# Performance work log

Measured on AMD Instinct MI355X. Metric: run time of the kernel, lower is better.

Reference implementation:

```python
import jax, jax.numpy as jnp
import numpy as np
import math

INPUT_DIM = 1024
DIM_K = 1024
DIM_V = 1024
B, N = 4, 2048

def setup_inputs() -> dict:
    key = jax.random.key(0)
    ks = jax.random.split(key, 7)
    s = 1.0 / math.sqrt(INPUT_DIM)
    return {
        'x':  jax.random.normal(ks[0], (B, N, INPUT_DIM), dtype=jnp.float32),
        'Wq': jax.random.uniform(ks[1], (DIM_K, INPUT_DIM), jnp.float32, -s, s),
        'bq': jax.random.uniform(ks[2], (DIM_K,), jnp.float32, -s, s),
        'Wk': jax.random.uniform(ks[3], (DIM_K, INPUT_DIM), jnp.float32, -s, s),
        'bk': jax.random.uniform(ks[4], (DIM_K,), jnp.float32, -s, s),
        'Wv': jax.random.uniform(ks[5], (DIM_V, INPUT_DIM), jnp.float32, -s, s),
        'bv': jax.random.uniform(ks[6], (DIM_V,), jnp.float32, -s, s),
    }

def reference(x, Wq, bq, Wk, bk, Wv, bv):
    norm_fact = 1.0 / math.sqrt(DIM_K)
    # torch Linear: y = x @ W.T + b
    Q = jnp.einsum('bnd,kd->bnk', x, Wq) + bq  # [B,N,dim_k]
    K = jnp.einsum('bnd,kd->bnk', x, Wk) + bk  # [B,N,dim_k]
    V = jnp.einsum('bnd,vd->bnv', x, Wv) + bv  # [B,N,dim_v]
    scores = jnp.einsum('bqk,bnk->bqn', Q, K)  # [B,N,N]
    # NOTE: original code applies softmax FIRST, then scales by norm_fact
    atten = jax.nn.softmax(scores, axis=-1) * norm_fact
    return jnp.einsum('bqn,bnv->bqv', atten, V)  # [B,N,dim_v]
```

## Files before the change

kernel.cpp:

```cpp
#include <hip/hip_runtime.h>


typedef _Float16 hfx8 __attribute__((ext_vector_type(8)));
typedef _Float16 hfx4 __attribute__((ext_vector_type(4)));
typedef float fx4 __attribute__((ext_vector_type(4)));

__device__ __forceinline__ void load_lds16(const void* g, void* l) {
    __builtin_amdgcn_global_load_lds(
        (const __attribute__((address_space(1))) void*)g,
        (__attribute__((address_space(3))) void*)l, 16, 0, 0);
}

template <int N> __device__ __forceinline__ void vmwait() {
    if constexpr (N == 8) asm volatile("s_waitcnt vmcnt(8)" ::: "memory");
    else if constexpr (N == 4) asm volatile("s_waitcnt vmcnt(4)" ::: "memory");
    else asm volatile("s_waitcnt vmcnt(0)" ::: "memory");
}

__device__ __forceinline__ void xcd_remap(int& x, int& y, int& z) {
    const int gx = gridDim.x, gy = gridDim.y;
    const int lin = blockIdx.x + gx * (blockIdx.y + gy * blockIdx.z);
    const int cpx = (gx * gy * gridDim.z) >> 3;
    const int w = (lin & 7) * cpx + (lin >> 3);
    x = w % gx;
    y = (w / gx) % gy;
    z = w / (gx * gy);
}

__global__ __launch_bounds__(256) void convx_kernel(
    const float4* __restrict__ in, _Float16* __restrict__ out)
{
    const int i = blockIdx.x * 256 + threadIdx.x;
    float4 v = in[i];
    hfx4 h;
    h[0] = (_Float16)v.x; h[1] = (_Float16)v.y;
    h[2] = (_Float16)v.z; h[3] = (_Float16)v.w;
    *(hfx4*)&out[(long)i * 4] = h;
}

__global__ __launch_bounds__(256) void convw3_kernel(
    const float4* __restrict__ w0, const float4* __restrict__ w1, const float4* __restrict__ w2,
    _Float16* __restrict__ o0, _Float16* __restrict__ o1, _Float16* __restrict__ o2)
{
    const int wsel = blockIdx.x >> 10;
    const float4* in = wsel == 0 ? w0 : (wsel == 1 ? w1 : w2);
    _Float16* out = wsel == 0 ? o0 : (wsel == 1 ? o1 : o2);
    const int i = (blockIdx.x & 1023) * 256 + threadIdx.x;
    float4 v = in[i];
    hfx4 h;
    h[0] = (_Float16)v.x; h[1] = (_Float16)v.y;
    h[2] = (_Float16)v.z; h[3] = (_Float16)v.w;
    *(hfx4*)&out[(long)i * 4] = h;
}

template <int OMODE>
__global__ __launch_bounds__(256, 4) void gemm2(
    const _Float16* __restrict__ A,
    const _Float16* __restrict__ Bq, const _Float16* __restrict__ Bk, const _Float16* __restrict__ Bv,
    const float* __restrict__ bq, const float* __restrict__ bk, const float* __restrict__ bv,
    float* __restrict__ outF, _Float16* __restrict__ oQ, _Float16* __restrict__ oK, _Float16* __restrict__ oV,
    int K, int lda, int ldb, int ldc, float alpha,
    long sAz, long sBz, long sCz)
{
    constexpr int BM = 128, BN = 128, BK = 32;
    constexpr int LPT = 4;

    __shared__ __attribute__((aligned(16))) _Float16 lds[2][(BM + BN) * BK];

    int bx, by, z;
    xcd_remap(bx, by, z);

    A += (long)z * sAz;
    const _Float16* B = (OMODE == 1) ? (z == 0 ? Bq : (z == 1 ? Bk : Bv))
                                     : Bq + (long)z * sBz;

    const int tid = threadIdx.x;
    const int lane = tid & 63;
    const int wv = tid >> 6;
    const int wr = wv >> 1, wc = wv & 1;
    const int lr = lane & 15, lk = lane >> 4;

    const long m0 = (long)by * BM;
    const long n0 = (long)bx * BN;

    fx4 acc[4][4] = {};

    auto STAGE = [&](int kt, int b) {
#pragma unroll
        for (int i = 0; i < LPT; ++i) {
            const int c = i * 256 + tid;
            if (i < 2) {
                const int row = c >> 2, slot = c & 3;
                load_lds16(A + (m0 + row) * (long)lda + kt + ((slot ^ ((row >> 1) & 3)) << 3),
                           &lds[b][row * 32 + slot * 8]);
            } else {
                const int c2 = c - 512;
                const int row = c2 >> 2, slot = c2 & 3;
                load_lds16(B + (n0 + row) * (long)ldb + kt + ((slot ^ ((row >> 1) & 3)) << 3),
                           &lds[b][BM * BK + row * 32 + slot * 8]);
            }
        }
    };

    const int NT = K / BK;
    STAGE(0, 0);
    STAGE(BK, 1);
    vmwait<4>();
    __builtin_amdgcn_s_barrier();
    __builtin_amdgcn_sched_barrier(0);

    const int rA0 = wr * 64 + lr;
    const int rB0 = wc * 64 + lr;
    const int eA = (((rA0 >> 1) & 3) << 3);
    const int eB = (((rB0 >> 1) & 3) << 3);

    for (int t = 0; t < NT; ++t) {
        const _Float16* LA = &lds[t & 1][0];
        const _Float16* LB = LA + BM * BK;

        hfx8 bfr[4];
#pragma unroll
        for (int nf = 0; nf < 4; ++nf)
            bfr[nf] = *(const hfx8*)&LB[(rB0 + nf * 16) * BK + ((lk * 8) ^ eB)];

#pragma unroll
        for (int q = 0; q < 4; ++q) {
            hfx8 afr = *(const hfx8*)&LA[(rA0 + q * 16) * BK + ((lk * 8) ^ eA)];
            __builtin_amdgcn_s_setprio(1);
#pragma unroll
            for (int nf = 0; nf < 4; ++nf)
                acc[q][nf] = __builtin_amdgcn_mfma_f32_16x16x32_f16(
                    afr, bfr[nf], acc[q][nf], 0, 0, 0);
            __builtin_amdgcn_s_setprio(0);
        }

        __builtin_amdgcn_s_barrier();
        if (t + 2 < NT) {
            STAGE((t + 2) * BK, t & 1);
            vmwait<4>();
        } else {
            vmwait<0>();
        }
        __builtin_amdgcn_s_barrier();
        __builtin_amdgcn_sched_barrier(0);
    }

#pragma unroll
    for (int mf = 0; mf < 4; ++mf) {
#pragma unroll
        for (int nf = 0; nf < 4; ++nf) {
            const long row0 = m0 + wr * 64 + mf * 16 + lk * 4;
            const long col = n0 + wc * 64 + nf * 16 + lr;
            if constexpr (OMODE == 0) {
                float* oz = outF + (long)z * sCz;
#pragma unroll
                for (int j = 0; j < 4; ++j)
                    oz[(row0 + j) * (long)ldc + col] = alpha * acc[mf][nf][j];
            } else {
                if (z == 0) {
                    const float bb = bq[col];
#pragma unroll
                    for (int j = 0; j < 4; ++j)
                        oQ[(row0 + j) * 1024 + col] = (_Float16)(acc[mf][nf][j] + bb);
                } else if (z == 1) {
                    const float bb = bk[col];
#pragma unroll
                    for (int j = 0; j < 4; ++j)
                        oK[(row0 + j) * 1024 + col] = (_Float16)(acc[mf][nf][j] + bb);
                } else {
                    const float bb = bv[col];
                    hfx4 pk;
#pragma unroll
                    for (int j = 0; j < 4; ++j) pk[j] = (_Float16)(acc[mf][nf][j] + bb);
                    *(hfx4*)&oV[((row0 >> 11) * 1024 + col) * 2048 + (row0 & 2047)] = pk;
                }
            }
        }
    }
}

__global__ __launch_bounds__(256) void softmax_kernel(float* __restrict__ S)
{
    const long row = blockIdx.x;
    float* r = S + row * 2048;
    const int t = threadIdx.x;

    float4 v0 = *(const float4*)&r[t * 4];
    float4 v1 = *(const float4*)&r[1024 + t * 4];
    float v[8] = {v0.x, v0.y, v0.z, v0.w, v1.x, v1.y, v1.z, v1.w};

    float mx = v[0];
#pragma unroll
    for (int j = 1; j < 8; ++j) mx = fmaxf(mx, v[j]);
#pragma unroll
    for (int o = 32; o; o >>= 1) mx = fmaxf(mx, __shfl_xor(mx, o, 64));

    __shared__ float redm[4];
    __shared__ float reds[4];
    const int w = t >> 6;
    if ((t & 63) == 0) redm[w] = mx;
    __syncthreads();
    mx = fmaxf(fmaxf(redm[0], redm[1]), fmaxf(redm[2], redm[3]));

    float e[8];
    float s = 0.f;
#pragma unroll
    for (int j = 0; j < 8; ++j) {
        e[j] = __expf(v[j] - mx);
        s += e[j];
    }
#pragma unroll
    for (int o = 32; o; o >>= 1) s += __shfl_xor(s, o, 64);
    if ((t & 63) == 0) reds[w] = s;
    __syncthreads();
    s = reds[0] + reds[1] + reds[2] + reds[3];

    const float inv = 1.0f / s;
    hfx4 p0, p1;
#pragma unroll
    for (int j = 0; j < 4; ++j) {
        p0[j] = (_Float16)(e[j] * inv);
        p1[j] = (_Float16)(e[4 + j] * inv);
    }
    _Float16* pr = (_Float16*)r;
    *(hfx4*)&pr[t * 4] = p0;
    *(hfx4*)&pr[1024 + t * 4] = p1;
}

extern "C" void kernel_launch(void* const* d_in, const int* in_sizes, int n_in,
                              void* d_out, int out_size, void* d_ws, size_t ws_size,
                              hipStream_t stream)
{
    const float* x  = (const float*)d_in[0];
    const float* Wq = (const float*)d_in[1];
    const float* bq = (const float*)d_in[2];
    const float* Wk = (const float*)d_in[3];
    const float* bk = (const float*)d_in[4];
    const float* Wv = (const float*)d_in[5];
    const float* bv = (const float*)d_in[6];
    float* out = (float*)d_out;

    _Float16* xs  = (_Float16*)d_ws;
    _Float16* Wqh = xs + 8192ull * 1024;
    _Float16* Wkh = Wqh + 1024ull * 1024;
    _Float16* Wvh = Wkh + 1024ull * 1024;
    _Float16* Qp  = Wvh + 1024ull * 1024;
    _Float16* Ks  = Qp + 8192ull * 1024;
    _Float16* Vt  = Ks + 8192ull * 1024;
    float* S      = (float*)(Vt + 4ull * 1024 * 2048);

    dim3 blk(256);

    convx_kernel<<<8192, blk, 0, stream>>>((const float4*)x, xs);
    convw3_kernel<<<3072, blk, 0, stream>>>(
        (const float4*)Wq, (const float4*)Wk, (const float4*)Wv, Wqh, Wkh, Wvh);

    gemm2<1><<<dim3(8, 64, 3), blk, 0, stream>>>(
        xs, Wqh, Wkh, Wvh, bq, bk, bv,
        nullptr, Qp, Ks, Vt,
        1024, 1024, 1024, 0, 1.0f, 0L, 0L, 0L);

    gemm2<0><<<dim3(16, 16, 4), blk, 0, stream>>>(
        Qp, Ks, nullptr, nullptr, nullptr, nullptr, nullptr,
        S, nullptr, nullptr, nullptr,
        1024, 1024, 1024, 2048, 1.0f,
        2097152L, 2097152L, 4194304L);

    softmax_kernel<<<2048 * 4, blk, 0, stream>>>(S);

    gemm2<0><<<dim3(8, 16, 4), blk, 0, stream>>>(
        (const _Float16*)S, Vt, nullptr, nullptr, nullptr, nullptr, nullptr,
        out, nullptr, nullptr, nullptr,
        2048, 4096, 2048, 1024, 0.03125f,
        8388608L, 2097152L, 2097152L);
}
```

Measured before the change: 190.0 us.

## Enlarge GEMM tile to 256x128 and merge conversion kernels

The GEMM tile grows from 128x128 to 256x128. Each wave now computes 128x64 with 8x4 MFMA accumulators, all A fragments are loaded before the MFMA loop, and the grids are halved along M. The change aims to raise arithmetic intensity per LDS and global load and to cut the number of blocks. The cost is higher register pressure and occupancy lowered to 2 blocks per CU, plus fewer blocks to fill 256 CUs. The x and weight fp32-to-fp16 conversion kernels are also fused into one launch to remove one kernel launch.

Result: no change. 190.3 us (+0.2%).

```diff
diff --git a/kernel.cpp b/kernel.cpp
--- a/kernel.cpp
+++ b/kernel.cpp
@@ -13,6 +13,7 @@
 
 template <int N> __device__ __forceinline__ void vmwait() {
     if constexpr (N == 8) asm volatile("s_waitcnt vmcnt(8)" ::: "memory");
+    else if constexpr (N == 6) asm volatile("s_waitcnt vmcnt(6)" ::: "memory");
     else if constexpr (N == 4) asm volatile("s_waitcnt vmcnt(4)" ::: "memory");
     else asm volatile("s_waitcnt vmcnt(0)" ::: "memory");
 }
@@ -27,34 +28,34 @@
     z = w / (gx * gy);
 }
 
-__global__ __launch_bounds__(256) void convx_kernel(
-    const float4* __restrict__ in, _Float16* __restrict__ out)
-{
-    const int i = blockIdx.x * 256 + threadIdx.x;
+__global__ __launch_bounds__(256) void conv_all_kernel(
+    const float4* __restrict__ x, _Float16* __restrict__ xs,
+    const float4* __restrict__ w0, const float4* __restrict__ w1, const float4* __restrict__ w2,
+    _Float16* __restrict__ o0, _Float16* __restrict__ o1, _Float16* __restrict__ o2)
+{
+    const int b = blockIdx.x;
+    const float4* in;
+    _Float16* out;
+    long i;
+    if (b < 8192) {
+        in = x; out = xs;
+        i = (long)b * 256 + threadIdx.x;
+    } else {
+        const int wi = b - 8192;
+        const int wsel = wi >> 10;
+        in = wsel == 0 ? w0 : (wsel == 1 ? w1 : w2);
+        out = wsel == 0 ? o0 : (wsel == 1 ? o1 : o2);
+        i = (long)(wi & 1023) * 256 + threadIdx.x;
+    }
     float4 v = in[i];
     hfx4 h;
     h[0] = (_Float16)v.x; h[1] = (_Float16)v.y;
     h[2] = (_Float16)v.z; h[3] = (_Float16)v.w;
-    *(hfx4*)&out[(long)i * 4] = h;
-}
-
-__global__ __launch_bounds__(256) void convw3_kernel(
-    const float4* __restrict__ w0, const float4* __restrict__ w1, const float4* __restrict__ w2,
-    _Float16* __restrict__ o0, _Float16* __restrict__ o1, _Float16* __restrict__ o2)
-{
-    const int wsel = blockIdx.x >> 10;
-    const float4* in = wsel == 0 ? w0 : (wsel == 1 ? w1 : w2);
-    _Float16* out = wsel == 0 ? o0 : (wsel == 1 ? o1 : o2);
-    const int i = (blockIdx.x & 1023) * 256 + threadIdx.x;
-    float4 v = in[i];
-    hfx4 h;
-    h[0] = (_Float16)v.x; h[1] = (_Float16)v.y;
-    h[2] = (_Float16)v.z; h[3] = (_Float16)v.w;
-    *(hfx4*)&out[(long)i * 4] = h;
+    *(hfx4*)&out[i * 4] = h;
 }
 
 template <int OMODE>
-__global__ __launch_bounds__(256, 4) void gemm2(
+__global__ __launch_bounds__(256, 2) void gemm3(
     const _Float16* __restrict__ A,
     const _Float16* __restrict__ Bq, const _Float16* __restrict__ Bk, const _Float16* __restrict__ Bv,
     const float* __restrict__ bq, const float* __restrict__ bk, const float* __restrict__ bv,
@@ -62,8 +63,8 @@
     int K, int lda, int ldb, int ldc, float alpha,
     long sAz, long sBz, long sCz)
 {
-    constexpr int BM = 128, BN = 128, BK = 32;
-    constexpr int LPT = 4;
+    constexpr int BM = 256, BN = 128, BK = 32;
+    constexpr int LPT = 6;
 
     __shared__ __attribute__((aligned(16))) _Float16 lds[2][(BM + BN) * BK];
 
@@ -83,18 +84,18 @@
     const long m0 = (long)by * BM;
     const long n0 = (long)bx * BN;
 
-    fx4 acc[4][4] = {};
+    fx4 acc[8][4] = {};
 
     auto STAGE = [&](int kt, int b) {
 #pragma unroll
         for (int i = 0; i < LPT; ++i) {
             const int c = i * 256 + tid;
-            if (i < 2) {
+            if (i < 4) {
                 const int row = c >> 2, slot = c & 3;
                 load_lds16(A + (m0 + row) * (long)lda + kt + ((slot ^ ((row >> 1) & 3)) << 3),
                            &lds[b][row * 32 + slot * 8]);
             } else {
-                const int c2 = c - 512;
+                const int c2 = c - 1024;
                 const int row = c2 >> 2, slot = c2 & 3;
                 load_lds16(B + (n0 + row) * (long)ldb + kt + ((slot ^ ((row >> 1) & 3)) << 3),
                            &lds[b][BM * BK + row * 32 + slot * 8]);
@@ -105,11 +106,11 @@
     const int NT = K / BK;
     STAGE(0, 0);
     STAGE(BK, 1);
-    vmwait<4>();
+    vmwait<6>();
     __builtin_amdgcn_s_barrier();
     __builtin_amdgcn_sched_barrier(0);
 
-    const int rA0 = wr * 64 + lr;
+    const int rA0 = wr * 128 + lr;
     const int rB0 = wc * 64 + lr;
     const int eA = (((rA0 >> 1) & 3) << 3);
     const int eB = (((rB0 >> 1) & 3) << 3);
@@ -122,22 +123,24 @@
 #pragma unroll
         for (int nf = 0; nf < 4; ++nf)
             bfr[nf] = *(const hfx8*)&LB[(rB0 + nf * 16) * BK + ((lk * 8) ^ eB)];
-
-#pragma unroll
-        for (int q = 0; q < 4; ++q) {
-            hfx8 afr = *(const hfx8*)&LA[(rA0 + q * 16) * BK + ((lk * 8) ^ eA)];
-            __builtin_amdgcn_s_setprio(1);
+        hfx8 afr[8];
+#pragma unroll
+        for (int mf = 0; mf < 8; ++mf)
+            afr[mf] = *(const hfx8*)&LA[(rA0 + mf * 16) * BK + ((lk * 8) ^ eA)];
+
+        __builtin_amdgcn_s_setprio(1);
+#pragma unroll
+        for (int mf = 0; mf < 8; ++mf)
 #pragma unroll
             for (int nf = 0; nf < 4; ++nf)
-                acc[q][nf] = __builtin_amdgcn_mfma_f32_16x16x32_f16(
-                    afr, bfr[nf], acc[q][nf], 0, 0, 0);
-            __builtin_amdgcn_s_setprio(0);
-        }
+                acc[mf][nf] = __builtin_amdgcn_mfma_f32_16x16x32_f16(
+                    afr[mf], bfr[nf], acc[mf][nf], 0, 0, 0);
+        __builtin_amdgcn_s_setprio(0);
 
         __builtin_amdgcn_s_barrier();
         if (t + 2 < NT) {
             STAGE((t + 2) * BK, t & 1);
-            vmwait<4>();
+            vmwait<6>();
         } else {
             vmwait<0>();
         }
@@ -146,10 +149,10 @@
     }
 
 #pragma unroll
-    for (int mf = 0; mf < 4; ++mf) {
+    for (int mf = 0; mf < 8; ++mf) {
 #pragma unroll
         for (int nf = 0; nf < 4; ++nf) {
-            const long row0 = m0 + wr * 64 + mf * 16 + lk * 4;
+            const long row0 = m0 + wr * 128 + mf * 16 + lk * 4;
             const long col = n0 + wc * 64 + nf * 16 + lr;
             if constexpr (OMODE == 0) {
                 float* oz = outF + (long)z * sCz;
@@ -251,16 +254,16 @@
 
     dim3 blk(256);
 
-    convx_kernel<<<8192, blk, 0, stream>>>((const float4*)x, xs);
-    convw3_kernel<<<3072, blk, 0, stream>>>(
+    conv_all_kernel<<<11264, blk, 0, stream>>>(
+        (const float4*)x, xs,
         (const float4*)Wq, (const float4*)Wk, (const float4*)Wv, Wqh, Wkh, Wvh);
 
-    gemm2<1><<<dim3(8, 64, 3), blk, 0, stream>>>(
+    gemm3<1><<<dim3(8, 32, 3), blk, 0, stream>>>(
         xs, Wqh, Wkh, Wvh, bq, bk, bv,
         nullptr, Qp, Ks, Vt,
         1024, 1024, 1024, 0, 1.0f, 0L, 0L, 0L);
 
-    gemm2<0><<<dim3(16, 16, 4), blk, 0, stream>>>(
+    gemm3<0><<<dim3(16, 8, 4), blk, 0, stream>>>(
         Qp, Ks, nullptr, nullptr, nullptr, nullptr, nullptr,
         S, nullptr, nullptr, nullptr,
         1024, 1024, 1024, 2048, 1.0f,
@@ -268,7 +271,7 @@
 
     softmax_kernel<<<2048 * 4, blk, 0, stream>>>(S);
 
-    gemm2<0><<<dim3(8, 16, 4), blk, 0, stream>>>(
+    gemm3<0><<<dim3(8, 8, 4), blk, 0, stream>>>(
         (const _Float16*)S, Vt, nullptr, nullptr, nullptr, nullptr, nullptr,
         out, nullptr, nullptr, nullptr,
         2048, 4096, 2048, 1024, 0.03125f,
```
